# Optimization experiments

Hardware: AMD Instinct MI355X
Metric: run time of the kernel (lower is better)

## Reference

```python
import jax, jax.numpy as jnp
import numpy as np

EPS = 1e-6
H, A, V = 4, 64, 64  # heads, attn_dim, hidden_dim


def layer_norm(x, w, b):
    mu = jnp.mean(x, axis=-1, keepdims=True)
    var = jnp.var(x, axis=-1, keepdims=True)
    return (x - mu) * jax.lax.rsqrt(var + EPS) * w + b


def setup_inputs() -> dict:
    key = jax.random.key(0)
    B, N, D = 4, 2048, 512
    lengths = np.array([2048, 1536, 1024, 1792], np.int32)
    offsets = np.concatenate([[0], np.cumsum(lengths)]).astype(np.int32)
    L = int(offsets[-1])  # 6400
    uvqk_out = (2 * V + 2 * A) * H  # 1024
    out_in = 2 * V * H + D          # concat([u, x, normed_attn])
    ks = jax.random.split(key, 4)
    return {
        "x": jax.random.normal(ks[0], (L, D), jnp.float32),
        "x_lengths": jnp.asarray(lengths),
        "x_offsets": jnp.asarray(offsets),
        "max_seq_len": N,
        "num_targets": jnp.asarray([32, 16, 8, 64], jnp.int32),
        "uvqk_weight": jax.random.normal(ks[1], (D, uvqk_out), jnp.float32) / np.float32(np.sqrt(D)),
        "uvqk_bias": jnp.zeros((uvqk_out,), jnp.float32),
        "input_norm_weight": jnp.ones((D,), jnp.float32),
        "input_norm_bias": jnp.zeros((D,), jnp.float32),
        "output_norm_weight": jnp.ones((V * H,), jnp.float32),
        "output_norm_bias": jnp.zeros((V * H,), jnp.float32),
        "output_weight": jax.random.normal(ks[2], (out_in, D), jnp.float32) / np.float32(np.sqrt(out_in)),
    }


def reference(x, x_lengths, x_offsets, max_seq_len, num_targets,
              uvqk_weight, uvqk_bias, input_norm_weight, input_norm_bias,
              output_norm_weight, output_norm_bias, output_weight):
    L, D = x.shape
    B = x_lengths.shape[0]
    N = int(max_seq_len)
    alpha = A ** -0.5

    # fused input layernorm + UVQK projection + silu
    nx = layer_norm(x, input_norm_weight, input_norm_bias)
    uvqk = jax.nn.silu(nx @ uvqk_weight + uvqk_bias)              # [L, (2V+2A)*H]
    u = uvqk[:, : V * H]                                          # [L, V*H]
    v = uvqk[:, V * H: 2 * V * H].reshape(L, H, V)
    q = uvqk[:, 2 * V * H: 2 * V * H + A * H].reshape(L, H, A)
    k = uvqk[:, 2 * V * H + A * H:].reshape(L, H, A)

    # jagged -> padded [B, N, ...]
    pos = jnp.arange(N)
    gather_idx = jnp.clip(x_offsets[:-1, None] + pos[None, :], 0, L - 1)  # [B,N]
    valid = pos[None, :] < x_lengths[:, None]                              # [B,N]
    qp = q[gather_idx] * valid[..., None, None]
    kp = k[gather_idx] * valid[..., None, None]
    vp = v[gather_idx] * valid[..., None, None]

    # target-aware causal mask: clamp ids at uih boundary; eye | dist>0
    max_ids = (x_lengths - num_targets)[:, None]        # [B,1]
    ids = jnp.minimum(pos[None, :], max_ids)            # [B,N]
    dist = ids[:, :, None] - ids[:, None, :]            # [B,N,N]
    mask = (dist > 0) | jnp.eye(N, dtype=bool)[None]
    mask = mask & valid[:, :, None] & valid[:, None, :]

    scores = jnp.einsum("bnha,bmha->bhnm", qp, kp) * alpha
    attn_w = jax.nn.silu(scores) * (1.0 / N)
    attn_w = attn_w * mask[:, None].astype(attn_w.dtype)
    attn_p = jnp.einsum("bhnm,bmhv->bnhv", attn_w, vp).reshape(B, N, H * V)

    # padded -> jagged
    tok = jnp.arange(L)
    b_of = jnp.searchsorted(x_offsets, tok, side="right") - 1
    p_of = tok - x_offsets[b_of]
    attn = attn_p[b_of, p_of]                            # [L, H*V]

    # output: norm(attn), concat [u, x, y], project, residual (dropout off / eval)
    y = layer_norm(attn, output_norm_weight, output_norm_bias)
    y = jnp.concatenate([u, x, y], axis=1)
    return x + y @ output_weight
```

## Files before the change

### kernel.cpp

```cpp
#include <hip/hip_runtime.h>
#include <math.h>

#define NSEQ 2048
#define PIT 72

typedef __attribute__((ext_vector_type(8))) short short8;
typedef __attribute__((ext_vector_type(4))) short short4v;
typedef __attribute__((ext_vector_type(4))) float f32x4;

__device__ __forceinline__ float silu_f(float z) {
    return z * __builtin_amdgcn_rcpf(1.f + __expf(-z));
}

__device__ __forceinline__ unsigned short f2bf(float f) {
    unsigned int u = __float_as_uint(f);
    u += 0x7fffu + ((u >> 16) & 1u);
    return (unsigned short)(u >> 16);
}

__device__ __forceinline__ unsigned short f2bf_fast(float f) {
    return (unsigned short)((__float_as_uint(f) + 0x8000u) >> 16);
}

__device__ __forceinline__ short8 scale8_pow2(short8 v, float s) {
    short8 r;
    #pragma unroll
    for (int i = 0; i < 8; i++) {
        float f = __uint_as_float(((unsigned int)(unsigned short)v[i]) << 16) * s;
        r[i] = (short)(unsigned short)(__float_as_uint(f) >> 16);
    }
    return r;
}

__global__ void __launch_bounds__(256) prep_kernel(
    const float* __restrict__ W1, unsigned short* __restrict__ W1t,
    const float* __restrict__ W2, unsigned short* __restrict__ W2t,
    const float* __restrict__ x, const float* __restrict__ inw,
    const float* __restrict__ inb,
    unsigned short* __restrict__ nxb, unsigned short* __restrict__ A2)
{
    __shared__ float t[32][33];
    int id = blockIdx.x;
    int tid = threadIdx.x;
    if (id < 1024) {
        const float* W; unsigned short* Wt; int R, C, bx, by;
        if (id < 512) { W = W1; Wt = W1t; R = 512;  C = 1024; bx = id & 31; by = id >> 5; }
        else { int i2 = id - 512; W = W2; Wt = W2t; R = 1024; C = 512; bx = i2 & 15; by = i2 >> 4; }
        int tr = tid >> 5, tc = tid & 31;
        int r0 = by * 32, c0 = bx * 32;
        #pragma unroll
        for (int p = 0; p < 4; p++)
            t[tr + p * 8][tc] = W[(size_t)(r0 + tr + p * 8) * C + c0 + tc];
        __syncthreads();
        #pragma unroll
        for (int p = 0; p < 4; p++)
            Wt[(size_t)(c0 + tr + p * 8) * R + r0 + tc] = f2bf(t[tc][tr + p * 8]);
        return;
    }
    int lane = tid & 63, wv = tid >> 6;
    int row = (id - 1024) * 4 + wv;
    int c = lane * 8;
    const float* xr = x + (size_t)row * 512 + c;
    float4 v0 = *(const float4*)xr;
    float4 v1 = *(const float4*)(xr + 4);
    float s  = v0.x + v0.y + v0.z + v0.w + v1.x + v1.y + v1.z + v1.w;
    float sq = v0.x * v0.x + v0.y * v0.y + v0.z * v0.z + v0.w * v0.w
             + v1.x * v1.x + v1.y * v1.y + v1.z * v1.z + v1.w * v1.w;
    #pragma unroll
    for (int o = 32; o > 0; o >>= 1) { s += __shfl_xor(s, o); sq += __shfl_xor(sq, o); }
    float mu = s * (1.f / 512.f);
    float var = sq * (1.f / 512.f) - mu * mu;
    float rs = rsqrtf(var + 1e-6f);
    float4 w0 = *(const float4*)(inw + c), w1 = *(const float4*)(inw + c + 4);
    float4 b0 = *(const float4*)(inb + c), b1 = *(const float4*)(inb + c + 4);
    ushort4 hn0, hn1, hx0, hx1;
    hn0.x = f2bf((v0.x - mu) * rs * w0.x + b0.x);
    hn0.y = f2bf((v0.y - mu) * rs * w0.y + b0.y);
    hn0.z = f2bf((v0.z - mu) * rs * w0.z + b0.z);
    hn0.w = f2bf((v0.w - mu) * rs * w0.w + b0.w);
    hn1.x = f2bf((v1.x - mu) * rs * w1.x + b1.x);
    hn1.y = f2bf((v1.y - mu) * rs * w1.y + b1.y);
    hn1.z = f2bf((v1.z - mu) * rs * w1.z + b1.z);
    hn1.w = f2bf((v1.w - mu) * rs * w1.w + b1.w);
    hx0.x = f2bf(v0.x); hx0.y = f2bf(v0.y); hx0.z = f2bf(v0.z); hx0.w = f2bf(v0.w);
    hx1.x = f2bf(v1.x); hx1.y = f2bf(v1.y); hx1.z = f2bf(v1.z); hx1.w = f2bf(v1.w);
    unsigned short* nr = nxb + (size_t)row * 512 + c;
    *(ushort4*)nr = hn0; *(ushort4*)(nr + 4) = hn1;
    unsigned short* ar = A2 + (size_t)row * 1024 + 256 + c;
    *(ushort4*)ar = hx0; *(ushort4*)(ar + 4) = hx1;
}

__global__ void __launch_bounds__(256) ln256_kernel(
    const float* __restrict__ a, const float* __restrict__ w,
    const float* __restrict__ b, unsigned short* __restrict__ A2)
{
    int tid = threadIdx.x, lane = tid & 63, wv = tid >> 6;
    int row = blockIdx.x * 4 + wv;
    int c = lane * 4;
    float4 v = *(const float4*)(a + (size_t)row * 256 + c);
    float s  = v.x + v.y + v.z + v.w;
    float sq = v.x * v.x + v.y * v.y + v.z * v.z + v.w * v.w;
    #pragma unroll
    for (int o = 32; o > 0; o >>= 1) { s += __shfl_xor(s, o); sq += __shfl_xor(sq, o); }
    float mu = s * (1.f / 256.f);
    float var = sq * (1.f / 256.f) - mu * mu;
    float rs = rsqrtf(var + 1e-6f);
    float4 w4 = *(const float4*)(w + c);
    float4 b4 = *(const float4*)(b + c);
    ushort4 h;
    h.x = f2bf((v.x - mu) * rs * w4.x + b4.x);
    h.y = f2bf((v.y - mu) * rs * w4.y + b4.y);
    h.z = f2bf((v.z - mu) * rs * w4.z + b4.z);
    h.w = f2bf((v.w - mu) * rs * w4.w + b4.w);
    *(ushort4*)(A2 + (size_t)row * 1024 + 768 + c) = h;
}

__global__ void __launch_bounds__(256) gemm1_mfma(
    const unsigned short* __restrict__ Ab, const unsigned short* __restrict__ Bt,
    const float* __restrict__ bias,
    unsigned short* __restrict__ A2, unsigned short* __restrict__ qkvb)
{
    constexpr int K = 512, KIT = K / 64;
    __shared__ unsigned short As[64 * PIT];
    __shared__ unsigned short Bs[64 * PIT];
    int p = blockIdx.x;
    int l = (p & 7) * 200 + (p >> 3);
    int bm = (l >> 4) * 64, bn = (l & 15) * 64;
    int tid = threadIdx.x, lane = tid & 63, w = tid >> 6;
    int wr = w >> 1, wc = w & 1;
    int nn = lane & 15, qd = lane >> 4;
    int arow = tid >> 2, ac0 = (tid & 3) * 16;
    const unsigned short* Ag = Ab + (size_t)(bm + arow) * K + ac0;
    const unsigned short* Bg = Bt + (size_t)(bn + arow) * K + ac0;

    short8 pa0 = *(const short8*)Ag, pa1 = *(const short8*)(Ag + 8);
    short8 pb0 = *(const short8*)Bg, pb1 = *(const short8*)(Bg + 8);

    f32x4 acc[2][2];
    #pragma unroll
    for (int i = 0; i < 2; i++)
        #pragma unroll
        for (int j = 0; j < 2; j++) acc[i][j] = (f32x4){0.f, 0.f, 0.f, 0.f};

    for (int it = 0; it < KIT; ++it) {
        __syncthreads();
        *(short8*)&As[arow * PIT + ac0]     = pa0;
        *(short8*)&As[arow * PIT + ac0 + 8] = pa1;
        *(short8*)&Bs[arow * PIT + ac0]     = pb0;
        *(short8*)&Bs[arow * PIT + ac0 + 8] = pb1;
        __syncthreads();
        if (it + 1 < KIT) {
            int k0 = (it + 1) * 64;
            pa0 = *(const short8*)(Ag + k0); pa1 = *(const short8*)(Ag + k0 + 8);
            pb0 = *(const short8*)(Bg + k0); pb1 = *(const short8*)(Bg + k0 + 8);
        }
        #pragma unroll
        for (int kk = 0; kk < 2; kk++) {
            short8 af[2], bf[2];
            #pragma unroll
            for (int i = 0; i < 2; i++)
                af[i] = *(const short8*)&As[(wr * 32 + i * 16 + nn) * PIT + kk * 32 + qd * 8];
            #pragma unroll
            for (int j = 0; j < 2; j++)
                bf[j] = *(const short8*)&Bs[(wc * 32 + j * 16 + nn) * PIT + kk * 32 + qd * 8];
            #pragma unroll
            for (int i = 0; i < 2; i++)
                #pragma unroll
                for (int j = 0; j < 2; j++)
                    acc[i][j] = __builtin_amdgcn_mfma_f32_16x16x32_bf16(af[i], bf[j], acc[i][j], 0, 0, 0);
        }
    }
    bool isU = (bn < 256);
    #pragma unroll
    for (int j = 0; j < 2; j++) {
        int col = bn + wc * 32 + j * 16 + nn;
        float bb = bias[col];
        #pragma unroll
        for (int i = 0; i < 2; i++) {
            int rbase = bm + wr * 32 + i * 16 + qd * 4;
            #pragma unroll
            for (int r = 0; r < 4; r++) {
                unsigned short hh = f2bf(silu_f(acc[i][j][r] + bb));
                if (isU) A2[(size_t)(rbase + r) * 1024 + col] = hh;
                else     qkvb[(size_t)(rbase + r) * 768 + col - 256] = hh;
            }
        }
    }
}

__global__ void __launch_bounds__(256) gemm2_mfma(
    const unsigned short* __restrict__ Ab, const unsigned short* __restrict__ Bt,
    const float* __restrict__ x, float* __restrict__ out)
{
    constexpr int K = 1024, KIT = K / 64;
    __shared__ unsigned short As[64 * PIT];
    __shared__ unsigned short Bs[64 * PIT];
    int p = blockIdx.x;
    int l = (p & 7) * 100 + (p >> 3);
    int bm = (l >> 3) * 64, bn = (l & 7) * 64;
    int tid = threadIdx.x, lane = tid & 63, w = tid >> 6;
    int wr = w >> 1, wc = w & 1;
    int nn = lane & 15, qd = lane >> 4;
    int arow = tid >> 2, ac0 = (tid & 3) * 16;
    const unsigned short* Ag = Ab + (size_t)(bm + arow) * K + ac0;
    const unsigned short* Bg = Bt + (size_t)(bn + arow) * K + ac0;

    short8 pa0 = *(const short8*)Ag, pa1 = *(const short8*)(Ag + 8);
    short8 pb0 = *(const short8*)Bg, pb1 = *(const short8*)(Bg + 8);

    f32x4 acc[2][2];
    #pragma unroll
    for (int i = 0; i < 2; i++)
        #pragma unroll
        for (int j = 0; j < 2; j++) acc[i][j] = (f32x4){0.f, 0.f, 0.f, 0.f};

    for (int it = 0; it < KIT; ++it) {
        __syncthreads();
        *(short8*)&As[arow * PIT + ac0]     = pa0;
        *(short8*)&As[arow * PIT + ac0 + 8] = pa1;
        *(short8*)&Bs[arow * PIT + ac0]     = pb0;
        *(short8*)&Bs[arow * PIT + ac0 + 8] = pb1;
        __syncthreads();
        if (it + 1 < KIT) {
            int k0 = (it + 1) * 64;
            pa0 = *(const short8*)(Ag + k0); pa1 = *(const short8*)(Ag + k0 + 8);
            pb0 = *(const short8*)(Bg + k0); pb1 = *(const short8*)(Bg + k0 + 8);
        }
        #pragma unroll
        for (int kk = 0; kk < 2; kk++) {
            short8 af[2], bf[2];
            #pragma unroll
            for (int i = 0; i < 2; i++)
                af[i] = *(const short8*)&As[(wr * 32 + i * 16 + nn) * PIT + kk * 32 + qd * 8];
            #pragma unroll
            for (int j = 0; j < 2; j++)
                bf[j] = *(const short8*)&Bs[(wc * 32 + j * 16 + nn) * PIT + kk * 32 + qd * 8];
            #pragma unroll
            for (int i = 0; i < 2; i++)
                #pragma unroll
                for (int j = 0; j < 2; j++)
                    acc[i][j] = __builtin_amdgcn_mfma_f32_16x16x32_bf16(af[i], bf[j], acc[i][j], 0, 0, 0);
        }
    }
    #pragma unroll
    for (int j = 0; j < 2; j++) {
        int col = bn + wc * 32 + j * 16 + nn;
        #pragma unroll
        for (int i = 0; i < 2; i++) {
            int rbase = bm + wr * 32 + i * 16 + qd * 4;
            #pragma unroll
            for (int r = 0; r < 4; r++) {
                size_t idx = (size_t)(rbase + r) * 512 + col;
                out[idx] = x[idx] + acc[i][j][r];
            }
        }
    }
}

__global__ void __launch_bounds__(256, 2) attn_mfma_kernel(
    const unsigned short* __restrict__ qkvb,
    const int* __restrict__ offsets,
    const int* __restrict__ lengths,
    const int* __restrict__ num_targets,
    float* __restrict__ attn)
{
    int id = blockIdx.x;
    int bh = id & 15;
    int xt = id >> 4;
    int b = bh >> 2, h = bh & 3;
    int len = lengths[b];
    int n0 = (31 - xt) * 64;
    if (n0 >= len) return;
    int m_hi = min(n0 + 63, len - 1);
    int off = offsets[b];
    int max_id = len - num_targets[b];
    int tid = threadIdx.x, lane = tid & 63, w = tid >> 6;
    int nn = lane & 15, qd = lane >> 4;

    __shared__ __align__(16) char smem[69632];
    unsigned short* Vt = (unsigned short*)(smem + w * 9216);
    float* Os = (float*)smem;

    short8 qf[4][2];
    #pragma unroll
    for (int g = 0; g < 4; g++) {
        int row = min(n0 + g * 16 + nn, len - 1);
        const unsigned short* base = qkvb + (size_t)(off + row) * 768 + 256 + h * 64;
        qf[g][0] = scale8_pow2(*(const short8*)(base + qd * 8), 0.125f);
        qf[g][1] = scale8_pow2(*(const short8*)(base + 32 + qd * 8), 0.125f);
    }

    f32x4 o_acc[4][4];
    #pragma unroll
    for (int t = 0; t < 4; t++)
        #pragma unroll
        for (int g = 0; g < 4; g++) o_acc[t][g] = (f32x4){0.f, 0.f, 0.f, 0.f};

    int fast_lim = min(n0, max_id);
    int r0 = (lane & 15) * 4, d0 = (lane >> 4) * 16;

    short8 kf[4][2], kn[4][2], vf[4][2];
    int m_first = w * 64;
    if (m_first <= m_hi) {
        #pragma unroll
        for (int s = 0; s < 4; s++) {
            int row = min(m_first + s * 16 + nn, len - 1);
            const unsigned short* kb = qkvb + (size_t)(off + row) * 768 + 512 + h * 64 + qd * 8;
            kf[s][0] = *(const short8*)kb;
            kf[s][1] = *(const short8*)(kb + 32);
        }
        #pragma unroll
        for (int j = 0; j < 4; j++) {
            int row = min(m_first + r0 + j, len - 1);
            const unsigned short* vb = qkvb + (size_t)(off + row) * 768 + h * 64 + d0;
            vf[j][0] = *(const short8*)vb;
            vf[j][1] = *(const short8*)(vb + 8);
        }
    }

    for (int m0 = m_first; m0 <= m_hi; m0 += 256) {
        #pragma unroll
        for (int dd = 0; dd < 16; dd++) {
            int hh = dd >> 3, e = dd & 7;
            short4v pk;
            pk[0] = vf[0][hh][e]; pk[1] = vf[1][hh][e];
            pk[2] = vf[2][hh][e]; pk[3] = vf[3][hh][e];
            *(short4v*)&Vt[(d0 + dd) * PIT + r0] = pk;
        }
        int mnext = m0 + 256;
        if (mnext <= m_hi) {
            #pragma unroll
            for (int j = 0; j < 4; j++) {
                int row = min(mnext + r0 + j, len - 1);
                const unsigned short* vb = qkvb + (size_t)(off + row) * 768 + h * 64 + d0;
                vf[j][0] = *(const short8*)vb;
                vf[j][1] = *(const short8*)(vb + 8);
            }
            #pragma unroll
            for (int s = 0; s < 4; s++) {
                int row = min(mnext + s * 16 + nn, len - 1);
                const unsigned short* kb = qkvb + (size_t)(off + row) * 768 + 512 + h * 64 + qd * 8;
                kn[s][0] = *(const short8*)kb;
                kn[s][1] = *(const short8*)(kb + 32);
            }
        }
        bool fastp = (m0 + 63 < fast_lim);
        #pragma unroll
        for (int s = 0; s < 4; s++) {
            f32x4 st[4];
            __builtin_amdgcn_s_setprio(1);
            #pragma unroll
            for (int g = 0; g < 4; g++) {
                st[g] = (f32x4){0.f, 0.f, 0.f, 0.f};
                st[g] = __builtin_amdgcn_mfma_f32_16x16x32_bf16(kf[s][0], qf[g][0], st[g], 0, 0, 0);
                st[g] = __builtin_amdgcn_mfma_f32_16x16x32_bf16(kf[s][1], qf[g][1], st[g], 0, 0, 0);
            }
            __builtin_amdgcn_s_setprio(0);
            short4v bop[4];
            if (fastp) {
                #pragma unroll
                for (int g = 0; g < 4; g++)
                    #pragma unroll
                    for (int r = 0; r < 4; r++)
                        bop[g][r] = (short)f2bf_fast(silu_f(st[g][r]));
            } else {
                #pragma unroll
                for (int g = 0; g < 4; g++) {
                    int nc_ = n0 + g * 16 + nn;
                    int id_ = min(nc_, max_id);
                    #pragma unroll
                    for (int r = 0; r < 4; r++) {
                        int mcol = m0 + s * 16 + qd * 4 + r;
                        bool ok = (mcol < id_) || (mcol == nc_);
                        bop[g][r] = (short)f2bf_fast(ok ? silu_f(st[g][r]) : 0.f);
                    }
                }
            }
            __builtin_amdgcn_s_setprio(1);
            #pragma unroll
            for (int t = 0; t < 4; t++) {
                short4v aop = *(const short4v*)&Vt[(t * 16 + nn) * PIT + s * 16 + qd * 4];
                #pragma unroll
                for (int g = 0; g < 4; g++)
                    o_acc[t][g] = __builtin_amdgcn_mfma_f32_16x16x16bf16_1k(aop, bop[g], o_acc[t][g], 0, 0, 0);
            }
            __builtin_amdgcn_s_setprio(0);
        }
        if (mnext <= m_hi) {
            #pragma unroll
            for (int s = 0; s < 4; s++) { kf[s][0] = kn[s][0]; kf[s][1] = kn[s][1]; }
        }
    }

    __syncthreads();
    const float invN = 1.f / (float)NSEQ;
    float* Ow = Os + w * 4352;
    #pragma unroll
    for (int t = 0; t < 4; t++)
        #pragma unroll
        for (int g = 0; g < 4; g++) {
            f32x4 v = o_acc[t][g] * invN;
            *(f32x4*)&Ow[(g * 16 + nn) * 68 + t * 16 + qd * 4] = v;
        }
    __syncthreads();
    int rr = tid >> 2, cs = (tid & 3) * 16;
    if (n0 + rr < len) {
        float* dst = attn + (size_t)(off + n0 + rr) * 256 + h * 64 + cs;
        #pragma unroll
        for (int q4 = 0; q4 < 4; q4++) {
            f32x4 v = (f32x4){0.f, 0.f, 0.f, 0.f};
            #pragma unroll
            for (int w2 = 0; w2 < 4; w2++)
                v += *(const f32x4*)&Os[w2 * 4352 + rr * 68 + cs + q4 * 4];
            *(f32x4*)(dst + q4 * 4) = v;
        }
    }
}

extern "C" void kernel_launch(void* const* d_in, const int* in_sizes, int n_in,
                              void* d_out, int out_size, void* d_ws, size_t ws_size,
                              hipStream_t stream)
{
    const float* x          = (const float*)d_in[0];
    const int*   x_lengths  = (const int*)d_in[1];
    const int*   x_offsets  = (const int*)d_in[2];
    const int*   num_targets = (const int*)d_in[4];
    const float* uvqk_w     = (const float*)d_in[5];
    const float* uvqk_b     = (const float*)d_in[6];
    const float* in_w       = (const float*)d_in[7];
    const float* in_b       = (const float*)d_in[8];
    const float* out_w      = (const float*)d_in[9];
    const float* out_b      = (const float*)d_in[10];
    const float* Wo         = (const float*)d_in[11];
    float* out = (float*)d_out;

    int L = in_sizes[0] / 512;

    char* ws = (char*)d_ws;
    size_t o = 0;
    float* attn = (float*)(ws + o);          o += (size_t)L * 256 * 4;
    unsigned short* nxb  = (unsigned short*)(ws + o); o += (size_t)L * 512 * 2;
    unsigned short* A2   = (unsigned short*)(ws + o); o += (size_t)L * 1024 * 2;
    unsigned short* qkvb = (unsigned short*)(ws + o); o += (size_t)L * 768 * 2;
    unsigned short* W1t  = (unsigned short*)(ws + o); o += (size_t)1024 * 512 * 2;
    unsigned short* W2t  = (unsigned short*)(ws + o); o += (size_t)512 * 1024 * 2;

    prep_kernel<<<dim3(1024 + L / 4), 256, 0, stream>>>(
        uvqk_w, W1t, Wo, W2t, x, in_w, in_b, nxb, A2);

    gemm1_mfma<<<dim3(1600), 256, 0, stream>>>(nxb, W1t, uvqk_b, A2, qkvb);

    attn_mfma_kernel<<<dim3(512), 256, 0, stream>>>(qkvb, x_offsets, x_lengths, num_targets, attn);

    ln256_kernel<<<L / 4, 256, 0, stream>>>(attn, out_w, out_b, A2);

    gemm2_mfma<<<dim3(800), 256, 0, stream>>>(A2, W2t, x, out);
}
```

Measured before the change: 158.8 us.

## Keep full B panel resident in LDS and stream A fragments from global

Both GEMMs now load an entire 64-column slice of the weight (the full K, or half of K for gemm2) into shared memory once per block. Each block then loops over several M tiles, reading A fragments straight from global memory into MFMA operands instead of staging them through LDS. The goal is to cut redundant weight reloads and per-k-step barriers, and to launch fewer, longer-lived blocks. The cost is much larger LDS use per block (about 66KB), which limits occupancy, and uncoalesced, unstaged global A loads that may add latency.

```diff
diff --git a/kernel.cpp b/kernel.cpp
--- a/kernel.cpp
+++ b/kernel.cpp
@@ -3,6 +3,7 @@
 
 #define NSEQ 2048
 #define PIT 72
+#define BPIT 520
 
 typedef __attribute__((ext_vector_type(8))) short short8;
 typedef __attribute__((ext_vector_type(4))) short short4v;
@@ -120,69 +121,63 @@
     const float* __restrict__ bias,
     unsigned short* __restrict__ A2, unsigned short* __restrict__ qkvb)
 {
-    constexpr int K = 512, KIT = K / 64;
-    __shared__ unsigned short As[64 * PIT];
-    __shared__ unsigned short Bs[64 * PIT];
+    constexpr int K = 512;
+    __shared__ unsigned short Bs[64 * BPIT];
     int p = blockIdx.x;
-    int l = (p & 7) * 200 + (p >> 3);
-    int bm = (l >> 4) * 64, bn = (l & 15) * 64;
+    int l = (p & 7) * 64 + (p >> 3);
+    int bnb = l >> 5, msub = l & 31;
+    int bn = bnb * 64;
     int tid = threadIdx.x, lane = tid & 63, w = tid >> 6;
     int wr = w >> 1, wc = w & 1;
     int nn = lane & 15, qd = lane >> 4;
-    int arow = tid >> 2, ac0 = (tid & 3) * 16;
-    const unsigned short* Ag = Ab + (size_t)(bm + arow) * K + ac0;
-    const unsigned short* Bg = Bt + (size_t)(bn + arow) * K + ac0;
-
-    short8 pa0 = *(const short8*)Ag, pa1 = *(const short8*)(Ag + 8);
-    short8 pb0 = *(const short8*)Bg, pb1 = *(const short8*)(Bg + 8);
-
-    f32x4 acc[2][2];
-    #pragma unroll
-    for (int i = 0; i < 2; i++)
-        #pragma unroll
-        for (int j = 0; j < 2; j++) acc[i][j] = (f32x4){0.f, 0.f, 0.f, 0.f};
-
-    for (int it = 0; it < KIT; ++it) {
-        __syncthreads();
-        *(short8*)&As[arow * PIT + ac0]     = pa0;
-        *(short8*)&As[arow * PIT + ac0 + 8] = pa1;
-        *(short8*)&Bs[arow * PIT + ac0]     = pb0;
-        *(short8*)&Bs[arow * PIT + ac0 + 8] = pb1;
-        __syncthreads();
-        if (it + 1 < KIT) {
-            int k0 = (it + 1) * 64;
-            pa0 = *(const short8*)(Ag + k0); pa1 = *(const short8*)(Ag + k0 + 8);
-            pb0 = *(const short8*)(Bg + k0); pb1 = *(const short8*)(Bg + k0 + 8);
-        }
-        #pragma unroll
-        for (int kk = 0; kk < 2; kk++) {
-            short8 af[2], bf[2];
-            #pragma unroll
-            for (int i = 0; i < 2; i++)
-                af[i] = *(const short8*)&As[(wr * 32 + i * 16 + nn) * PIT + kk * 32 + qd * 8];
-            #pragma unroll
-            for (int j = 0; j < 2; j++)
-                bf[j] = *(const short8*)&Bs[(wc * 32 + j * 16 + nn) * PIT + kk * 32 + qd * 8];
-            #pragma unroll
-            for (int i = 0; i < 2; i++)
+
+    {
+        int row = tid >> 2, c0 = (tid & 3) * 128;
+        const unsigned short* src = Bt + (size_t)(bn + row) * K + c0;
+        unsigned short* dst = &Bs[row * BPIT + c0];
+        #pragma unroll
+        for (int i = 0; i < 16; i++)
+            *(short8*)(dst + i * 8) = *(const short8*)(src + i * 8);
+    }
+    __syncthreads();
+
+    float bb[2];
+    int col0 = bn + wc * 32 + nn;
+    bb[0] = bias[col0]; bb[1] = bias[col0 + 16];
+    bool isU = (bn < 256);
+
+    for (int pm = msub; pm < 100; pm += 32) {
+        int bm = pm * 64;
+        const unsigned short* Ag = Ab + (size_t)(bm + wr * 32 + nn) * K + qd * 8;
+        f32x4 acc[2][2];
+        #pragma unroll
+        for (int i = 0; i < 2; i++)
+            #pragma unroll
+            for (int j = 0; j < 2; j++) acc[i][j] = (f32x4){0.f, 0.f, 0.f, 0.f};
+
+        #pragma unroll 8
+        for (int kk = 0; kk < 16; kk++) {
+            short8 af0 = *(const short8*)(Ag + kk * 32);
+            short8 af1 = *(const short8*)(Ag + 16 * K + kk * 32);
+            short8 bf0 = *(const short8*)&Bs[(wc * 32 + nn) * BPIT + kk * 32 + qd * 8];
+            short8 bf1 = *(const short8*)&Bs[(wc * 32 + 16 + nn) * BPIT + kk * 32 + qd * 8];
+            acc[0][0] = __builtin_amdgcn_mfma_f32_16x16x32_bf16(af0, bf0, acc[0][0], 0, 0, 0);
+            acc[0][1] = __builtin_amdgcn_mfma_f32_16x16x32_bf16(af0, bf1, acc[0][1], 0, 0, 0);
+            acc[1][0] = __builtin_amdgcn_mfma_f32_16x16x32_bf16(af1, bf0, acc[1][0], 0, 0, 0);
+            acc[1][1] = __builtin_amdgcn_mfma_f32_16x16x32_bf16(af1, bf1, acc[1][1], 0, 0, 0);
+        }
+        #pragma unroll
+        for (int j = 0; j < 2; j++) {
+            int col = col0 + j * 16;
+            #pragma unroll
+            for (int i = 0; i < 2; i++) {
+                int rbase = bm + wr * 32 + i * 16 + qd * 4;
                 #pragma unroll
-                for (int j = 0; j < 2; j++)
-                    acc[i][j] = __builtin_amdgcn_mfma_f32_16x16x32_bf16(af[i], bf[j], acc[i][j], 0, 0, 0);
-        }
-    }
-    bool isU = (bn < 256);
-    #pragma unroll
-    for (int j = 0; j < 2; j++) {
-        int col = bn + wc * 32 + j * 16 + nn;
-        float bb = bias[col];
-        #pragma unroll
-        for (int i = 0; i < 2; i++) {
-            int rbase = bm + wr * 32 + i * 16 + qd * 4;
-            #pragma unroll
-            for (int r = 0; r < 4; r++) {
-                unsigned short hh = f2bf(silu_f(acc[i][j][r] + bb));
-                if (isU) A2[(size_t)(rbase + r) * 1024 + col] = hh;
-                else     qkvb[(size_t)(rbase + r) * 768 + col - 256] = hh;
+                for (int r = 0; r < 4; r++) {
+                    unsigned short hh = f2bf(silu_f(acc[i][j][r] + bb[j]));
+                    if (isU) A2[(size_t)(rbase + r) * 1024 + col] = hh;
+                    else     qkvb[(size_t)(rbase + r) * 768 + col - 256] = hh;
+                }
             }
         }
     }
@@ -192,66 +187,79 @@
     const unsigned short* __restrict__ Ab, const unsigned short* __restrict__ Bt,
     const float* __restrict__ x, float* __restrict__ out)
 {
-    constexpr int K = 1024, KIT = K / 64;
-    __shared__ unsigned short As[64 * PIT];
-    __shared__ unsigned short Bs[64 * PIT];
+    constexpr int K = 1024;
+    __shared__ unsigned short Bs[64 * BPIT];
     int p = blockIdx.x;
-    int l = (p & 7) * 100 + (p >> 3);
-    int bm = (l >> 3) * 64, bn = (l & 7) * 64;
+    int l = (p & 7) * 64 + (p >> 3);
+    int bnb = l >> 6, msub = l & 63;
+    int bn = bnb * 64;
     int tid = threadIdx.x, lane = tid & 63, w = tid >> 6;
     int wr = w >> 1, wc = w & 1;
     int nn = lane & 15, qd = lane >> 4;
-    int arow = tid >> 2, ac0 = (tid & 3) * 16;
-    const unsigned short* Ag = Ab + (size_t)(bm + arow) * K + ac0;
-    const unsigned short* Bg = Bt + (size_t)(bn + arow) * K + ac0;
-
-    short8 pa0 = *(const short8*)Ag, pa1 = *(const short8*)(Ag + 8);
-    short8 pb0 = *(const short8*)Bg, pb1 = *(const short8*)(Bg + 8);
-
-    f32x4 acc[2][2];
+    int bm0 = msub * 64, bm1 = (msub + 64) * 64;
+    bool has2 = (msub + 64 < 100);
+
+    f32x4 acc0[2][2], acc1[2][2];
     #pragma unroll
     for (int i = 0; i < 2; i++)
         #pragma unroll
-        for (int j = 0; j < 2; j++) acc[i][j] = (f32x4){0.f, 0.f, 0.f, 0.f};
-
-    for (int it = 0; it < KIT; ++it) {
+        for (int j = 0; j < 2; j++) {
+            acc0[i][j] = (f32x4){0.f, 0.f, 0.f, 0.f};
+            acc1[i][j] = (f32x4){0.f, 0.f, 0.f, 0.f};
+        }
+
+    int srow = tid >> 2, sc0 = (tid & 3) * 128;
+
+    #define G2_PANEL(ACC, BM)                                                          \
+    {                                                                                  \
+        const unsigned short* Ag = Ab + (size_t)((BM) + wr * 32 + nn) * K              \
+                                   + c * 512 + qd * 8;                                 \
+        _Pragma("unroll 4")                                                            \
+        for (int kk = 0; kk < 16; kk++) {                                              \
+            short8 af0 = *(const short8*)(Ag + kk * 32);                               \
+            short8 af1 = *(const short8*)(Ag + 16 * K + kk * 32);                      \
+            short8 bf0 = *(const short8*)&Bs[(wc * 32 + nn) * BPIT + kk * 32 + qd * 8];      \
+            short8 bf1 = *(const short8*)&Bs[(wc * 32 + 16 + nn) * BPIT + kk * 32 + qd * 8]; \
+            ACC[0][0] = __builtin_amdgcn_mfma_f32_16x16x32_bf16(af0, bf0, ACC[0][0], 0, 0, 0); \
+            ACC[0][1] = __builtin_amdgcn_mfma_f32_16x16x32_bf16(af0, bf1, ACC[0][1], 0, 0, 0); \
+            ACC[1][0] = __builtin_amdgcn_mfma_f32_16x16x32_bf16(af1, bf0, ACC[1][0], 0, 0, 0); \
+            ACC[1][1] = __builtin_amdgcn_mfma_f32_16x16x32_bf16(af1, bf1, ACC[1][1], 0, 0, 0); \
+        }                                                                              \
+    }
+
+    for (int c = 0; c < 2; c++) {
+        if (c) __syncthreads();
+        {
+            const unsigned short* src = Bt + (size_t)(bn + srow) * K + c * 512 + sc0;
+            unsigned short* dst = &Bs[srow * BPIT + sc0];
+            #pragma unroll
+            for (int i = 0; i < 16; i++)
+                *(short8*)(dst + i * 8) = *(const short8*)(src + i * 8);
+        }
         __syncthreads();
-        *(short8*)&As[arow * PIT + ac0]     = pa0;
-        *(short8*)&As[arow * PIT + ac0 + 8] = pa1;
-        *(short8*)&Bs[arow * PIT + ac0]     = pb0;
-        *(short8*)&Bs[arow * PIT + ac0 + 8] = pb1;
-        __syncthreads();
-        if (it + 1 < KIT) {
-            int k0 = (it + 1) * 64;
-            pa0 = *(const short8*)(Ag + k0); pa1 = *(const short8*)(Ag + k0 + 8);
-            pb0 = *(const short8*)(Bg + k0); pb1 = *(const short8*)(Bg + k0 + 8);
-        }
-        #pragma unroll
-        for (int kk = 0; kk < 2; kk++) {
-            short8 af[2], bf[2];
-            #pragma unroll
-            for (int i = 0; i < 2; i++)
-                af[i] = *(const short8*)&As[(wr * 32 + i * 16 + nn) * PIT + kk * 32 + qd * 8];
-            #pragma unroll
-            for (int j = 0; j < 2; j++)
-                bf[j] = *(const short8*)&Bs[(wc * 32 + j * 16 + nn) * PIT + kk * 32 + qd * 8];
-            #pragma unroll
-            for (int i = 0; i < 2; i++)
-                #pragma unroll
-                for (int j = 0; j < 2; j++)
-                    acc[i][j] = __builtin_amdgcn_mfma_f32_16x16x32_bf16(af[i], bf[j], acc[i][j], 0, 0, 0);
-        }
-    }
+        G2_PANEL(acc0, bm0)
+        if (has2) G2_PANEL(acc1, bm1)
+    }
+    #undef G2_PANEL
+
     #pragma unroll
     for (int j = 0; j < 2; j++) {
         int col = bn + wc * 32 + j * 16 + nn;
         #pragma unroll
         for (int i = 0; i < 2; i++) {
-            int rbase = bm + wr * 32 + i * 16 + qd * 4;
+            int rb0 = bm0 + wr * 32 + i * 16 + qd * 4;
             #pragma unroll
             for (int r = 0; r < 4; r++) {
-                size_t idx = (size_t)(rbase + r) * 512 + col;
-                out[idx] = x[idx] + acc[i][j][r];
+                size_t idx = (size_t)(rb0 + r) * 512 + col;
+                out[idx] = x[idx] + acc0[i][j][r];
+            }
+            if (has2) {
+                int rb1 = bm1 + wr * 32 + i * 16 + qd * 4;
+                #pragma unroll
+                for (int r = 0; r < 4; r++) {
+                    size_t idx = (size_t)(rb1 + r) * 512 + col;
+                    out[idx] = x[idx] + acc1[i][j][r];
+                }
             }
         }
     }
@@ -448,11 +456,11 @@
     prep_kernel<<<dim3(1024 + L / 4), 256, 0, stream>>>(
         uvqk_w, W1t, Wo, W2t, x, in_w, in_b, nxb, A2);
 
-    gemm1_mfma<<<dim3(1600), 256, 0, stream>>>(nxb, W1t, uvqk_b, A2, qkvb);
+    gemm1_mfma<<<dim3(512), 256, 0, stream>>>(nxb, W1t, uvqk_b, A2, qkvb);
 
     attn_mfma_kernel<<<dim3(512), 256, 0, stream>>>(qkvb, x_offsets, x_lengths, num_targets, attn);
 
     ln256_kernel<<<L / 4, 256, 0, stream>>>(attn, out_w, out_b, A2);
 
-    gemm2_mfma<<<dim3(800), 256, 0, stream>>>(A2, W2t, x, out);
-}
+    gemm2_mfma<<<dim3(512), 256, 0, stream>>>(A2, W2t, x, out);
+}
```

New measurement: 204.2 us. +28.6%, slower.

## Use direct global-to-LDS loads with XOR swizzle and double buffering in GEMMs

Applied to the files above, without the earlier changes.

Both projection GEMMs now stage A and B tiles with global_load_lds 16-byte transfers straight into a double-buffered, XOR-swizzled LDS layout. This replaces register-staged prefetch with padded rows and cuts one barrier per K step. The weight transpose in the prep kernel also reads float4 vectors instead of scalars. The price is doubled LDS per block and reliance on the async load finishing before the single barrier, with no explicit vmcnt wait shown.

```diff
diff --git a/kernel.cpp b/kernel.cpp
--- a/kernel.cpp
+++ b/kernel.cpp
@@ -30,6 +30,12 @@
         r[i] = (short)(unsigned short)(__float_as_uint(f) >> 16);
     }
     return r;
+}
+
+__device__ __forceinline__ void gload16(const unsigned short* g, unsigned short* l) {
+    __builtin_amdgcn_global_load_lds(
+        (const __attribute__((address_space(1))) unsigned short*)g,
+        (__attribute__((address_space(3))) unsigned short*)l, 16, 0, 0);
 }
 
 __global__ void __launch_bounds__(256) prep_kernel(
@@ -46,12 +52,12 @@
         const float* W; unsigned short* Wt; int R, C, bx, by;
         if (id < 512) { W = W1; Wt = W1t; R = 512;  C = 1024; bx = id & 31; by = id >> 5; }
         else { int i2 = id - 512; W = W2; Wt = W2t; R = 1024; C = 512; bx = i2 & 15; by = i2 >> 4; }
+        int r0 = by * 32, c0 = bx * 32;
+        int rr = tid >> 3, cc = (tid & 7) * 4;
+        float4 v = *(const float4*)(W + (size_t)(r0 + rr) * C + c0 + cc);
+        t[rr][cc] = v.x; t[rr][cc + 1] = v.y; t[rr][cc + 2] = v.z; t[rr][cc + 3] = v.w;
+        __syncthreads();
         int tr = tid >> 5, tc = tid & 31;
-        int r0 = by * 32, c0 = bx * 32;
-        #pragma unroll
-        for (int p = 0; p < 4; p++)
-            t[tr + p * 8][tc] = W[(size_t)(r0 + tr + p * 8) * C + c0 + tc];
-        __syncthreads();
         #pragma unroll
         for (int p = 0; p < 4; p++)
             Wt[(size_t)(c0 + tr + p * 8) * R + r0 + tc] = f2bf(t[tc][tr + p * 8]);
@@ -115,26 +121,28 @@
     *(ushort4*)(A2 + (size_t)row * 1024 + 768 + c) = h;
 }
 
+
 __global__ void __launch_bounds__(256) gemm1_mfma(
     const unsigned short* __restrict__ Ab, const unsigned short* __restrict__ Bt,
     const float* __restrict__ bias,
     unsigned short* __restrict__ A2, unsigned short* __restrict__ qkvb)
 {
-    constexpr int K = 512, KIT = K / 64;
-    __shared__ unsigned short As[64 * PIT];
-    __shared__ unsigned short Bs[64 * PIT];
+    constexpr int K = 512, KIT = 8;
+    __shared__ unsigned short lds[16384];
     int p = blockIdx.x;
     int l = (p & 7) * 200 + (p >> 3);
     int bm = (l >> 4) * 64, bn = (l & 15) * 64;
     int tid = threadIdx.x, lane = tid & 63, w = tid >> 6;
     int wr = w >> 1, wc = w & 1;
     int nn = lane & 15, qd = lane >> 4;
-    int arow = tid >> 2, ac0 = (tid & 3) * 16;
-    const unsigned short* Ag = Ab + (size_t)(bm + arow) * K + ac0;
-    const unsigned short* Bg = Bt + (size_t)(bn + arow) * K + ac0;
-
-    short8 pa0 = *(const short8*)Ag, pa1 = *(const short8*)(Ag + 8);
-    short8 pb0 = *(const short8*)Bg, pb1 = *(const short8*)(Bg + 8);
+
+    int r8 = lane >> 3, u = lane & 7;
+    int su = ((u ^ r8) << 3);
+    int rA0 = w * 16;
+    const unsigned short* Asrc = Ab + (size_t)(bm + rA0 + r8) * K + su;
+    const unsigned short* Bsrc = Bt + (size_t)(bn + rA0 + r8) * K + su;
+
+    int fsw = nn & 7;
 
     f32x4 acc[2][2];
     #pragma unroll
@@ -142,34 +150,44 @@
         #pragma unroll
         for (int j = 0; j < 2; j++) acc[i][j] = (f32x4){0.f, 0.f, 0.f, 0.f};
 
+    gload16(Asrc,         &lds[rA0 * 64]);
+    gload16(Asrc + 8 * K, &lds[(rA0 + 8) * 64]);
+    gload16(Bsrc,         &lds[4096 + rA0 * 64]);
+    gload16(Bsrc + 8 * K, &lds[4096 + (rA0 + 8) * 64]);
+    __syncthreads();
+
     for (int it = 0; it < KIT; ++it) {
-        __syncthreads();
-        *(short8*)&As[arow * PIT + ac0]     = pa0;
-        *(short8*)&As[arow * PIT + ac0 + 8] = pa1;
-        *(short8*)&Bs[arow * PIT + ac0]     = pb0;
-        *(short8*)&Bs[arow * PIT + ac0 + 8] = pb1;
-        __syncthreads();
+        int cur = it & 1;
+        unsigned short* Asc = lds + cur * 8192;
+        unsigned short* Bsc = Asc + 4096;
         if (it + 1 < KIT) {
-            int k0 = (it + 1) * 64;
-            pa0 = *(const short8*)(Ag + k0); pa1 = *(const short8*)(Ag + k0 + 8);
-            pb0 = *(const short8*)(Bg + k0); pb1 = *(const short8*)(Bg + k0 + 8);
+            unsigned short* An = lds + (cur ^ 1) * 8192;
+            const unsigned short* a2 = Asrc + (it + 1) * 64;
+            const unsigned short* b2 = Bsrc + (it + 1) * 64;
+            gload16(a2,         &An[rA0 * 64]);
+            gload16(a2 + 8 * K, &An[(rA0 + 8) * 64]);
+            gload16(b2,         &An[4096 + rA0 * 64]);
+            gload16(b2 + 8 * K, &An[4096 + (rA0 + 8) * 64]);
         }
         #pragma unroll
         for (int kk = 0; kk < 2; kk++) {
+            int un = (((kk * 4 + qd) ^ fsw) << 3);
             short8 af[2], bf[2];
             #pragma unroll
             for (int i = 0; i < 2; i++)
-                af[i] = *(const short8*)&As[(wr * 32 + i * 16 + nn) * PIT + kk * 32 + qd * 8];
+                af[i] = *(const short8*)&Asc[(wr * 32 + i * 16 + nn) * 64 + un];
             #pragma unroll
             for (int j = 0; j < 2; j++)
-                bf[j] = *(const short8*)&Bs[(wc * 32 + j * 16 + nn) * PIT + kk * 32 + qd * 8];
+                bf[j] = *(const short8*)&Bsc[(wc * 32 + j * 16 + nn) * 64 + un];
             #pragma unroll
             for (int i = 0; i < 2; i++)
                 #pragma unroll
                 for (int j = 0; j < 2; j++)
                     acc[i][j] = __builtin_amdgcn_mfma_f32_16x16x32_bf16(af[i], bf[j], acc[i][j], 0, 0, 0);
         }
-    }
+        __syncthreads();
+    }
+
     bool isU = (bn < 256);
     #pragma unroll
     for (int j = 0; j < 2; j++) {
@@ -192,21 +210,22 @@
     const unsigned short* __restrict__ Ab, const unsigned short* __restrict__ Bt,
     const float* __restrict__ x, float* __restrict__ out)
 {
-    constexpr int K = 1024, KIT = K / 64;
-    __shared__ unsigned short As[64 * PIT];
-    __shared__ unsigned short Bs[64 * PIT];
+    constexpr int K = 1024, KIT = 16;
+    __shared__ unsigned short lds[16384];
     int p = blockIdx.x;
     int l = (p & 7) * 100 + (p >> 3);
     int bm = (l >> 3) * 64, bn = (l & 7) * 64;
     int tid = threadIdx.x, lane = tid & 63, w = tid >> 6;
     int wr = w >> 1, wc = w & 1;
     int nn = lane & 15, qd = lane >> 4;
-    int arow = tid >> 2, ac0 = (tid & 3) * 16;
-    const unsigned short* Ag = Ab + (size_t)(bm + arow) * K + ac0;
-    const unsigned short* Bg = Bt + (size_t)(bn + arow) * K + ac0;
-
-    short8 pa0 = *(const short8*)Ag, pa1 = *(const short8*)(Ag + 8);
-    short8 pb0 = *(const short8*)Bg, pb1 = *(const short8*)(Bg + 8);
+
+    int r8 = lane >> 3, u = lane & 7;
+    int su = ((u ^ r8) << 3);
+    int rA0 = w * 16;
+    const unsigned short* Asrc = Ab + (size_t)(bm + rA0 + r8) * K + su;
+    const unsigned short* Bsrc = Bt + (size_t)(bn + rA0 + r8) * K + su;
+
+    int fsw = nn & 7;
 
     f32x4 acc[2][2];
     #pragma unroll
@@ -214,34 +233,44 @@
         #pragma unroll
         for (int j = 0; j < 2; j++) acc[i][j] = (f32x4){0.f, 0.f, 0.f, 0.f};
 
+    gload16(Asrc,         &lds[rA0 * 64]);
+    gload16(Asrc + 8 * K, &lds[(rA0 + 8) * 64]);
+    gload16(Bsrc,         &lds[4096 + rA0 * 64]);
+    gload16(Bsrc + 8 * K, &lds[4096 + (rA0 + 8) * 64]);
+    __syncthreads();
+
     for (int it = 0; it < KIT; ++it) {
-        __syncthreads();
-        *(short8*)&As[arow * PIT + ac0]     = pa0;
-        *(short8*)&As[arow * PIT + ac0 + 8] = pa1;
-        *(short8*)&Bs[arow * PIT + ac0]     = pb0;
-        *(short8*)&Bs[arow * PIT + ac0 + 8] = pb1;
-        __syncthreads();
+        int cur = it & 1;
+        unsigned short* Asc = lds + cur * 8192;
+        unsigned short* Bsc = Asc + 4096;
         if (it + 1 < KIT) {
-            int k0 = (it + 1) * 64;
-            pa0 = *(const short8*)(Ag + k0); pa1 = *(const short8*)(Ag + k0 + 8);
-            pb0 = *(const short8*)(Bg + k0); pb1 = *(const short8*)(Bg + k0 + 8);
+            unsigned short* An = lds + (cur ^ 1) * 8192;
+            const unsigned short* a2 = Asrc + (it + 1) * 64;
+            const unsigned short* b2 = Bsrc + (it + 1) * 64;
+            gload16(a2,         &An[rA0 * 64]);
+            gload16(a2 + 8 * K, &An[(rA0 + 8) * 64]);
+            gload16(b2,         &An[4096 + rA0 * 64]);
+            gload16(b2 + 8 * K, &An[4096 + (rA0 + 8) * 64]);
         }
         #pragma unroll
         for (int kk = 0; kk < 2; kk++) {
+            int un = (((kk * 4 + qd) ^ fsw) << 3);
             short8 af[2], bf[2];
             #pragma unroll
             for (int i = 0; i < 2; i++)
-                af[i] = *(const short8*)&As[(wr * 32 + i * 16 + nn) * PIT + kk * 32 + qd * 8];
+                af[i] = *(const short8*)&Asc[(wr * 32 + i * 16 + nn) * 64 + un];
             #pragma unroll
             for (int j = 0; j < 2; j++)
-                bf[j] = *(const short8*)&Bs[(wc * 32 + j * 16 + nn) * PIT + kk * 32 + qd * 8];
+                bf[j] = *(const short8*)&Bsc[(wc * 32 + j * 16 + nn) * 64 + un];
             #pragma unroll
             for (int i = 0; i < 2; i++)
                 #pragma unroll
                 for (int j = 0; j < 2; j++)
                     acc[i][j] = __builtin_amdgcn_mfma_f32_16x16x32_bf16(af[i], bf[j], acc[i][j], 0, 0, 0);
         }
-    }
+        __syncthreads();
+    }
+
     #pragma unroll
     for (int j = 0; j < 2; j++) {
         int col = bn + wc * 32 + j * 16 + nn;
```

New measurement: 151.8 us. 4.4% less time.
